# Performance work log

Measured on AMD Instinct MI355X. Metric: run time of the kernel, lower is better.

Reference implementation:

```python
import jax, jax.numpy as jnp
import numpy as np

N, D, H, O, P = 50000, 256, 512, 64, 1024


def setup_inputs() -> dict:
    key = jax.random.key(0)
    ks = jax.random.split(key, 9)
    x = jax.random.normal(ks[0], (N, D), dtype=jnp.float32)
    W1 = jax.random.normal(ks[1], (H, D), dtype=jnp.float32) / np.sqrt(D)
    b1 = jax.random.normal(ks[2], (H,), dtype=jnp.float32) * 0.01
    W2 = jax.random.normal(ks[3], (O, H), dtype=jnp.float32) / np.sqrt(H)
    b2 = jax.random.normal(ks[4], (O,), dtype=jnp.float32) * 0.01
    ap = jax.random.randint(ks[5], (P,), 0, N, dtype=jnp.int32)
    p = jax.random.randint(ks[6], (P,), 0, N, dtype=jnp.int32)
    an = jax.random.randint(ks[7], (P,), 0, N, dtype=jnp.int32)
    n = jax.random.randint(ks[8], (P,), 0, N, dtype=jnp.int32)
    return {"x": x, "W1": W1, "b1": b1, "W2": W2, "b2": b2,
            "ap": ap, "p": p, "an": an, "n": n}


def reference(x, W1, b1, W2, b2, ap, p, an, n):
    """ContrastiveHessianCalculator.compute_hessian, loss_func='contrastive_full',
    wrt='weight', shape='diagonal', speed='half' (exact GGN diag), for the nnj net
    Linear(D,H) -> Tanh -> Linear(H,O).

    For a pair (x1,x2) the combined diag m0 - 2*m1 + m2 equals
    diag((J1-J2)^T (J1-J2)) where Ji = d f(xi)/d params. Closed form per layer:
      W1[i,j]: S11_i*x1_j^2 - 2*S12_i*x1_j*x2_j + S22_i*x2_j^2,
               Sab_i = tanh'(z1a)_i * tanh'(z1b)_i * sum_o W2[o,i]^2
      b1[i]:   S11_i - 2*S12_i + S22_i
      W2[i,j]: (h1_j - h2_j)^2  (independent of output row i)
      b2[i]:   0  (bias Jacobians of the two branches cancel)
    Per-layer diags are flattened [weight, bias] and concatenated (torch.cat(.., dim=1)),
    then summed over the pair batch; return sum(pos) - sum(neg).
    """
    c = jnp.sum(W2 * W2, axis=0)  # [H]

    def pair_hess_diag(ia, ib):
        xa = x[ia]            # [P, D]
        xb = x[ib]            # [P, D]
        ha = jnp.tanh(xa @ W1.T + b1)   # [P, H]
        hb = jnp.tanh(xb @ W1.T + b1)
        da = 1.0 - ha * ha              # tanh' at x_a, [P, H]
        db = 1.0 - hb * hb
        S11 = da * da * c               # [P, H]
        S12 = da * db * c
        S22 = db * db * c
        # W1 diag: [P, H, D]
        W1d = (S11[:, :, None] * (xa * xa)[:, None, :]
               - 2.0 * S12[:, :, None] * (xa * xb)[:, None, :]
               + S22[:, :, None] * (xb * xb)[:, None, :])
        b1d = S11 - 2.0 * S12 + S22      # [P, H]
        hd = (ha - hb) ** 2              # [P, H]
        W2d = jnp.broadcast_to(hd[:, None, :], (hd.shape[0], O, H))  # [P, O, H]
        b2d = jnp.zeros((hd.shape[0], O), dtype=hd.dtype)
        flat = jnp.concatenate([W1d.reshape(hd.shape[0], -1), b1d,
                                W2d.reshape(hd.shape[0], -1), b2d], axis=1)
        return jnp.sum(flat, axis=0)     # sum over pair batch -> [n_params]

    pos = pair_hess_diag(ap, p)
    neg = pair_hess_diag(an, n)
    return pos - neg
```

## Files before the change

### kernel.cpp

```cpp
#include <hip/hip_runtime.h>
#include <math.h>

#define DD_ 256
#define HH_ 512
#define OO_ 64

typedef __attribute__((ext_vector_type(8))) short bf16x8s;
typedef __attribute__((ext_vector_type(4))) float f32x4;

__device__ __forceinline__ unsigned short f2bf(float f) {
    unsigned u = __float_as_uint(f);
    u += 0x7FFF + ((u >> 16) & 1);
    return (unsigned short)(u >> 16);
}
__device__ __forceinline__ float bf2f(unsigned short h) {
    return __uint_as_float(((unsigned)h) << 16);
}
__device__ __forceinline__ void conv8(const float4& v0, const float4& v1,
                                      bf16x8s& hi, bf16x8s& lo) {
    float f[8] = {v0.x, v0.y, v0.z, v0.w, v1.x, v1.y, v1.z, v1.w};
    #pragma unroll
    for (int e = 0; e < 8; ++e) {
        unsigned short hh = f2bf(f[e]);
        hi[e] = (short)hh;
        lo[e] = (short)f2bf(f[e] - bf2f(hh));
    }
}
__device__ __forceinline__ int swz8(int r, int s) {
    return s ^ (r & 7);
}

__global__ __launch_bounds__(256) void k_mega(
    const float* __restrict__ x, const float* __restrict__ W1,
    const float* __restrict__ b1, const float* __restrict__ W2,
    const int* __restrict__ ap, const int* __restrict__ pI,
    const int* __restrict__ an, const int* __restrict__ nI,
    short* __restrict__ Mt, short* __restrict__ Xt,
    float* __restrict__ pb1, float* __restrict__ phd) {
    const int t = threadIdx.x;
    const int bb = blockIdx.x;
    if (bb < 512) {
        __shared__ short Ah[64 * 64], Al[64 * 64], Bh[64 * 64], Bl[64 * 64];
        __shared__ float ht[64][67];
        __shared__ int sidx[64];
        const int n0 = (bb & 7) * 64;
        const int ry = bb >> 3;
        const int s = ry >> 5;
        const int p0 = (ry & 31) * 32;
        const int* IA = s ? an : ap;
        const int* IB = s ? nI : pI;
        if (t < 32) sidx[t] = IA[p0 + t];
        else if (t < 64) sidx[t] = IB[p0 + t - 32];
        __syncthreads();
        const int row = t >> 2, q = t & 3;
        const int l = t & 63, w = t >> 6;
        const int wm = w >> 1, wn = w & 1;
        const int lm = l & 15, g = l >> 4;
        const int sl0 = swz8(row, 2 * q) * 8;
        const int sl1 = swz8(row, 2 * q + 1) * 8;
        const float* srcA = x + (size_t)sidx[row] * DD_ + q * 16;
        const float* srcB = W1 + (size_t)(n0 + row) * DD_ + q * 16;
        f32x4 acc[2][2] = {};
        for (int ks = 0; ks < 4; ++ks) {
            const int k0 = ks * 64;
            {
                float4 a0 = *(const float4*)(srcA + k0);
                float4 a1 = *(const float4*)(srcA + k0 + 4);
                float4 a2 = *(const float4*)(srcA + k0 + 8);
                float4 a3 = *(const float4*)(srcA + k0 + 12);
                bf16x8s hi, lo;
                conv8(a0, a1, hi, lo);
                *(bf16x8s*)(&Ah[row * 64 + sl0]) = hi;
                *(bf16x8s*)(&Al[row * 64 + sl0]) = lo;
                conv8(a2, a3, hi, lo);
                *(bf16x8s*)(&Ah[row * 64 + sl1]) = hi;
                *(bf16x8s*)(&Al[row * 64 + sl1]) = lo;
            }
            {
                float4 b0 = *(const float4*)(srcB + k0);
                float4 b1q = *(const float4*)(srcB + k0 + 4);
                float4 b2 = *(const float4*)(srcB + k0 + 8);
                float4 b3 = *(const float4*)(srcB + k0 + 12);
                bf16x8s hi, lo;
                conv8(b0, b1q, hi, lo);
                *(bf16x8s*)(&Bh[row * 64 + sl0]) = hi;
                *(bf16x8s*)(&Bl[row * 64 + sl0]) = lo;
                conv8(b2, b3, hi, lo);
                *(bf16x8s*)(&Bh[row * 64 + sl1]) = hi;
                *(bf16x8s*)(&Bl[row * 64 + sl1]) = lo;
            }
            __syncthreads();
            #pragma unroll
            for (int kk = 0; kk < 2; ++kk) {
                bf16x8s ah[2], al[2], bh[2], bl[2];
                #pragma unroll
                for (int mi = 0; mi < 2; ++mi) {
                    int r = wm * 32 + mi * 16 + lm;
                    int off = r * 64 + swz8(r, kk * 4 + g) * 8;
                    ah[mi] = *(const bf16x8s*)(&Ah[off]);
                    al[mi] = *(const bf16x8s*)(&Al[off]);
                }
                #pragma unroll
                for (int nj = 0; nj < 2; ++nj) {
                    int r = wn * 32 + nj * 16 + lm;
                    int off = r * 64 + swz8(r, kk * 4 + g) * 8;
                    bh[nj] = *(const bf16x8s*)(&Bh[off]);
                    bl[nj] = *(const bf16x8s*)(&Bl[off]);
                }
                #pragma unroll
                for (int mi = 0; mi < 2; ++mi)
                    #pragma unroll
                    for (int nj = 0; nj < 2; ++nj) {
                        acc[mi][nj] = __builtin_amdgcn_mfma_f32_16x16x32_bf16(ah[mi], bh[nj], acc[mi][nj], 0, 0, 0);
                        acc[mi][nj] = __builtin_amdgcn_mfma_f32_16x16x32_bf16(ah[mi], bl[nj], acc[mi][nj], 0, 0, 0);
                        acc[mi][nj] = __builtin_amdgcn_mfma_f32_16x16x32_bf16(al[mi], bh[nj], acc[mi][nj], 0, 0, 0);
                    }
            }
            __syncthreads();
        }
        #pragma unroll
        for (int mi = 0; mi < 2; ++mi)
            #pragma unroll
            for (int nj = 0; nj < 2; ++nj) {
                int jl = wn * 32 + nj * 16 + lm;
                float bv = b1[n0 + jl];
                #pragma unroll
                for (int qq = 0; qq < 4; ++qq) {
                    int r = wm * 32 + mi * 16 + g * 4 + qq;
                    ht[r][jl] = tanhf(acc[mi][nj][qq] + bv);
                }
            }
        __syncthreads();
        const int il = t >> 2, pq = t & 3;
        float ci = 0.f;
        #pragma unroll 8
        for (int o = 0; o < OO_; ++o) { float wv = W2[o * HH_ + n0 + il]; ci += wv * wv; }
        const float sgn = s ? -1.f : 1.f;
        float b1p = 0.f, hdp = 0.f;
        bf16x8s v0, v1, v2;
        #pragma unroll
        for (int pp = 0; pp < 8; ++pp) {
            int pl = pq * 8 + pp;
            float ha = ht[pl][il];
            float hb = ht[pl + 32][il];
            float da = 1.f - ha * ha, db = 1.f - hb * hb;
            float s11 = sgn * (da * da * ci);
            float s12 = sgn * (-2.f * da * db * ci);
            float s22 = sgn * (db * db * ci);
            v0[pp] = (short)f2bf(s11);
            v1[pp] = (short)f2bf(s12);
            v2[pp] = (short)f2bf(s22);
            b1p += s11 + s12 + s22;
            float d = ha - hb;
            hdp += sgn * d * d;
        }
        size_t base = (size_t)(n0 + il) * 6144 + s * 1024 + p0 + pq * 8;
        *(bf16x8s*)(&Mt[base]) = v0;
        *(bf16x8s*)(&Mt[base + 2048]) = v1;
        *(bf16x8s*)(&Mt[base + 4096]) = v2;
        b1p += __shfl_xor(b1p, 1); b1p += __shfl_xor(b1p, 2);
        hdp += __shfl_xor(hdp, 1); hdp += __shfl_xor(hdp, 2);
        if (pq == 0) { pb1[ry * HH_ + n0 + il] = b1p; phd[ry * HH_ + n0 + il] = hdp; }
    } else {
        __shared__ int sia[64], sib[64];
        const int b2 = bb - 512;
        const int jblk = b2 >> 5, pblk = b2 & 31;
        const int j = jblk * 64 + (t >> 2), pq = t & 3;
        const int p0 = pblk * 64;
        const int s = p0 >> 10;
        const int* IA = s ? an : ap;
        const int* IB = s ? nI : pI;
        if (t < 64) sia[t] = IA[(p0 & 1023) + t];
        else if (t < 128) sib[t - 64] = IB[(p0 & 1023) + (t - 64)];
        __syncthreads();
        short xv[3][16];
        #pragma unroll
        for (int pp = 0; pp < 16; ++pp) {
            int pl = pq * 16 + pp;
            float xa = x[(size_t)sia[pl] * DD_ + j];
            float xb = x[(size_t)sib[pl] * DD_ + j];
            xv[0][pp] = (short)f2bf(xa * xa);
            xv[1][pp] = (short)f2bf(xa * xb);
            xv[2][pp] = (short)f2bf(xb * xb);
        }
        size_t base = (size_t)j * 6144 + p0 + pq * 16;
        #pragma unroll
        for (int term = 0; term < 3; ++term) {
            bf16x8s v0, v1;
            #pragma unroll
            for (int e = 0; e < 8; ++e) { v0[e] = xv[term][e]; v1[e] = xv[term][e + 8]; }
            *(bf16x8s*)(&Xt[base + (size_t)term * 2048]) = v0;
            *(bf16x8s*)(&Xt[base + (size_t)term * 2048 + 8]) = v1;
        }
    }
}

__global__ __launch_bounds__(256) void k_gemm2(
    const short* __restrict__ Mt, const short* __restrict__ Xt,
    float* __restrict__ part) {
    __shared__ short As[64 * 64], Bs[64 * 64];
    const int t = threadIdx.x;
    const int j0 = blockIdx.x * 64;
    const int i0 = blockIdx.y * 64;
    const int kb = blockIdx.z;
    const int row = t >> 2, q = t & 3;
    const int l = t & 63, w = t >> 6;
    const int wm = w >> 1, wn = w & 1;
    const int lm = l & 15, g = l >> 4;
    const int sl0 = swz8(row, 2 * q) * 8;
    const int sl1 = swz8(row, 2 * q + 1) * 8;
    const short* srcA = &Mt[(size_t)(i0 + row) * 6144 + kb * 384 + q * 16];
    const short* srcB = &Xt[(size_t)(j0 + row) * 6144 + kb * 384 + q * 16];
    f32x4 acc[2][2] = {};
    for (int ks = 0; ks < 6; ++ks) {
        const int k0 = ks * 64;
        *(bf16x8s*)(&As[row * 64 + sl0]) = *(const bf16x8s*)(srcA + k0);
        *(bf16x8s*)(&As[row * 64 + sl1]) = *(const bf16x8s*)(srcA + k0 + 8);
        *(bf16x8s*)(&Bs[row * 64 + sl0]) = *(const bf16x8s*)(srcB + k0);
        *(bf16x8s*)(&Bs[row * 64 + sl1]) = *(const bf16x8s*)(srcB + k0 + 8);
        __syncthreads();
        #pragma unroll
        for (int kk = 0; kk < 2; ++kk) {
            bf16x8s a[2], b[2];
            #pragma unroll
            for (int mi = 0; mi < 2; ++mi) {
                int r = wm * 32 + mi * 16 + lm;
                a[mi] = *(const bf16x8s*)(&As[r * 64 + swz8(r, kk * 4 + g) * 8]);
            }
            #pragma unroll
            for (int nj = 0; nj < 2; ++nj) {
                int r = wn * 32 + nj * 16 + lm;
                b[nj] = *(const bf16x8s*)(&Bs[r * 64 + swz8(r, kk * 4 + g) * 8]);
            }
            #pragma unroll
            for (int mi = 0; mi < 2; ++mi)
                #pragma unroll
                for (int nj = 0; nj < 2; ++nj)
                    acc[mi][nj] = __builtin_amdgcn_mfma_f32_16x16x32_bf16(a[mi], b[nj], acc[mi][nj], 0, 0, 0);
        }
        __syncthreads();
    }
    #pragma unroll
    for (int mi = 0; mi < 2; ++mi)
        #pragma unroll
        for (int nj = 0; nj < 2; ++nj) {
            int j = j0 + wn * 32 + nj * 16 + lm;
            #pragma unroll
            for (int qq = 0; qq < 4; ++qq) {
                int i = i0 + wm * 32 + mi * 16 + g * 4 + qq;
                part[((size_t)kb * HH_ + i) * DD_ + j] = acc[mi][nj][qq];
            }
        }
}

__global__ void k_tail(const float* __restrict__ part, const float* __restrict__ pb1,
                       const float* __restrict__ phd, float* __restrict__ out) {
    int gid = blockIdx.x * 256 + threadIdx.x;
    const int HD = HH_ * DD_;
    if (gid < HD) {
        float sv = 0.f;
        #pragma unroll
        for (int kb = 0; kb < 16; ++kb) sv += part[(size_t)kb * HD + gid];
        out[gid] = sv;
    } else if (gid < HD + HH_) {
        int i = gid - HD;
        float sv = 0.f;
        #pragma unroll
        for (int kb = 0; kb < 64; ++kb) sv += pb1[kb * HH_ + i];
        out[gid] = sv;
    } else if (gid < HD + HH_ + OO_ * HH_) {
        int i = (gid - HD - HH_) & (HH_ - 1);
        float sv = 0.f;
        #pragma unroll
        for (int kb = 0; kb < 64; ++kb) sv += phd[kb * HH_ + i];
        out[gid] = sv;
    } else if (gid < HD + HH_ + OO_ * HH_ + OO_) {
        out[gid] = 0.f;
    }
}

extern "C" void kernel_launch(void* const* d_in, const int* in_sizes, int n_in,
                              void* d_out, int out_size, void* d_ws, size_t ws_size,
                              hipStream_t stream) {
    const float* x  = (const float*)d_in[0];
    const float* W1 = (const float*)d_in[1];
    const float* b1 = (const float*)d_in[2];
    const float* W2 = (const float*)d_in[3];
    const int* ap = (const int*)d_in[5];
    const int* pI = (const int*)d_in[6];
    const int* an = (const int*)d_in[7];
    const int* nI = (const int*)d_in[8];
    float* out = (float*)d_out;
    float* ws = (float*)d_ws;

    float* part = ws;
    short* Mt   = (short*)(ws + 2097152);
    short* Xt   = (short*)(ws + 3670016);
    float* pb1  = ws + 4456448;
    float* phd  = ws + 4489216;

    k_mega<<<dim3(640), dim3(256), 0, stream>>>(x, W1, b1, W2, ap, pI, an, nI,
                                                Mt, Xt, pb1, phd);
    k_gemm2<<<dim3(4, 8, 16), dim3(256), 0, stream>>>(Mt, Xt, part);
    k_tail<<<dim3(643), dim3(256), 0, stream>>>(part, pb1, phd, out);
}
```

Baseline: 31.78 us.

## Fold Xt build into mega blocks, double split-K, vectorize tail reduction

The separate 128 blocks that built the Xt (x products) operand are removed. Each of the 512 GEMM1 blocks now also writes a quarter of an Xt tile after its own work, so the launch is uniform and 512 blocks wide. The second GEMM's split-K factor doubles from 16 to 32, halving the K per block to get more blocks in flight. The tail now reduces with float4 vectors, and one thread writes all 64 replicated W2 rows per vector. The costs are more partial-sum traffic (32 slices), a larger workspace, and Xt gathers that now read indices from global memory without an LDS stage.

```diff
diff --git a/kernel.cpp b/kernel.cpp
--- a/kernel.cpp
+++ b/kernel.cpp
@@ -6,6 +6,7 @@
 #define OO_ 64
 
 typedef __attribute__((ext_vector_type(8))) short bf16x8s;
+typedef __attribute__((ext_vector_type(4))) short bf16x4s;
 typedef __attribute__((ext_vector_type(4))) float f32x4;
 
 __device__ __forceinline__ unsigned short f2bf(float f) {
@@ -37,100 +38,100 @@
     const int* __restrict__ an, const int* __restrict__ nI,
     short* __restrict__ Mt, short* __restrict__ Xt,
     float* __restrict__ pb1, float* __restrict__ phd) {
+    __shared__ short Ah[64 * 64], Al[64 * 64], Bh[64 * 64], Bl[64 * 64];
+    __shared__ float ht[64][67];
+    __shared__ int sidx[64];
     const int t = threadIdx.x;
     const int bb = blockIdx.x;
-    if (bb < 512) {
-        __shared__ short Ah[64 * 64], Al[64 * 64], Bh[64 * 64], Bl[64 * 64];
-        __shared__ float ht[64][67];
-        __shared__ int sidx[64];
-        const int n0 = (bb & 7) * 64;
-        const int ry = bb >> 3;
-        const int s = ry >> 5;
-        const int p0 = (ry & 31) * 32;
-        const int* IA = s ? an : ap;
-        const int* IB = s ? nI : pI;
-        if (t < 32) sidx[t] = IA[p0 + t];
-        else if (t < 64) sidx[t] = IB[p0 + t - 32];
+    const int n0 = (bb & 7) * 64;
+    const int ry = bb >> 3;
+    const int s = ry >> 5;
+    const int p0 = (ry & 31) * 32;
+    const int* IA = s ? an : ap;
+    const int* IB = s ? nI : pI;
+    if (t < 32) sidx[t] = IA[p0 + t];
+    else if (t < 64) sidx[t] = IB[p0 + t - 32];
+    __syncthreads();
+    const int row = t >> 2, q = t & 3;
+    const int l = t & 63, w = t >> 6;
+    const int wm = w >> 1, wn = w & 1;
+    const int lm = l & 15, g = l >> 4;
+    const int sl0 = swz8(row, 2 * q) * 8;
+    const int sl1 = swz8(row, 2 * q + 1) * 8;
+    const float* srcA = x + (size_t)sidx[row] * DD_ + q * 16;
+    const float* srcB = W1 + (size_t)(n0 + row) * DD_ + q * 16;
+    f32x4 acc[2][2] = {};
+    for (int ks = 0; ks < 4; ++ks) {
+        const int k0 = ks * 64;
+        {
+            float4 a0 = *(const float4*)(srcA + k0);
+            float4 a1 = *(const float4*)(srcA + k0 + 4);
+            float4 a2 = *(const float4*)(srcA + k0 + 8);
+            float4 a3 = *(const float4*)(srcA + k0 + 12);
+            bf16x8s hi, lo;
+            conv8(a0, a1, hi, lo);
+            *(bf16x8s*)(&Ah[row * 64 + sl0]) = hi;
+            *(bf16x8s*)(&Al[row * 64 + sl0]) = lo;
+            conv8(a2, a3, hi, lo);
+            *(bf16x8s*)(&Ah[row * 64 + sl1]) = hi;
+            *(bf16x8s*)(&Al[row * 64 + sl1]) = lo;
+        }
+        {
+            float4 b0 = *(const float4*)(srcB + k0);
+            float4 b1q = *(const float4*)(srcB + k0 + 4);
+            float4 b2 = *(const float4*)(srcB + k0 + 8);
+            float4 b3 = *(const float4*)(srcB + k0 + 12);
+            bf16x8s hi, lo;
+            conv8(b0, b1q, hi, lo);
+            *(bf16x8s*)(&Bh[row * 64 + sl0]) = hi;
+            *(bf16x8s*)(&Bl[row * 64 + sl0]) = lo;
+            conv8(b2, b3, hi, lo);
+            *(bf16x8s*)(&Bh[row * 64 + sl1]) = hi;
+            *(bf16x8s*)(&Bl[row * 64 + sl1]) = lo;
+        }
         __syncthreads();
-        const int row = t >> 2, q = t & 3;
-        const int l = t & 63, w = t >> 6;
-        const int wm = w >> 1, wn = w & 1;
-        const int lm = l & 15, g = l >> 4;
-        const int sl0 = swz8(row, 2 * q) * 8;
-        const int sl1 = swz8(row, 2 * q + 1) * 8;
-        const float* srcA = x + (size_t)sidx[row] * DD_ + q * 16;
-        const float* srcB = W1 + (size_t)(n0 + row) * DD_ + q * 16;
-        f32x4 acc[2][2] = {};
-        for (int ks = 0; ks < 4; ++ks) {
-            const int k0 = ks * 64;
-            {
-                float4 a0 = *(const float4*)(srcA + k0);
-                float4 a1 = *(const float4*)(srcA + k0 + 4);
-                float4 a2 = *(const float4*)(srcA + k0 + 8);
-                float4 a3 = *(const float4*)(srcA + k0 + 12);
-                bf16x8s hi, lo;
-                conv8(a0, a1, hi, lo);
-                *(bf16x8s*)(&Ah[row * 64 + sl0]) = hi;
-                *(bf16x8s*)(&Al[row * 64 + sl0]) = lo;
-                conv8(a2, a3, hi, lo);
-                *(bf16x8s*)(&Ah[row * 64 + sl1]) = hi;
-                *(bf16x8s*)(&Al[row * 64 + sl1]) = lo;
-            }
-            {
-                float4 b0 = *(const float4*)(srcB + k0);
-                float4 b1q = *(const float4*)(srcB + k0 + 4);
-                float4 b2 = *(const float4*)(srcB + k0 + 8);
-                float4 b3 = *(const float4*)(srcB + k0 + 12);
-                bf16x8s hi, lo;
-                conv8(b0, b1q, hi, lo);
-                *(bf16x8s*)(&Bh[row * 64 + sl0]) = hi;
-                *(bf16x8s*)(&Bl[row * 64 + sl0]) = lo;
-                conv8(b2, b3, hi, lo);
-                *(bf16x8s*)(&Bh[row * 64 + sl1]) = hi;
-                *(bf16x8s*)(&Bl[row * 64 + sl1]) = lo;
-            }
-            __syncthreads();
-            #pragma unroll
-            for (int kk = 0; kk < 2; ++kk) {
-                bf16x8s ah[2], al[2], bh[2], bl[2];
-                #pragma unroll
-                for (int mi = 0; mi < 2; ++mi) {
-                    int r = wm * 32 + mi * 16 + lm;
-                    int off = r * 64 + swz8(r, kk * 4 + g) * 8;
-                    ah[mi] = *(const bf16x8s*)(&Ah[off]);
-                    al[mi] = *(const bf16x8s*)(&Al[off]);
-                }
+        #pragma unroll
+        for (int kk = 0; kk < 2; ++kk) {
+            bf16x8s ah[2], al[2], bh[2], bl[2];
+            #pragma unroll
+            for (int mi = 0; mi < 2; ++mi) {
+                int r = wm * 32 + mi * 16 + lm;
+                int off = r * 64 + swz8(r, kk * 4 + g) * 8;
+                ah[mi] = *(const bf16x8s*)(&Ah[off]);
+                al[mi] = *(const bf16x8s*)(&Al[off]);
+            }
+            #pragma unroll
+            for (int nj = 0; nj < 2; ++nj) {
+                int r = wn * 32 + nj * 16 + lm;
+                int off = r * 64 + swz8(r, kk * 4 + g) * 8;
+                bh[nj] = *(const bf16x8s*)(&Bh[off]);
+                bl[nj] = *(const bf16x8s*)(&Bl[off]);
+            }
+            #pragma unroll
+            for (int mi = 0; mi < 2; ++mi)
                 #pragma unroll
                 for (int nj = 0; nj < 2; ++nj) {
-                    int r = wn * 32 + nj * 16 + lm;
-                    int off = r * 64 + swz8(r, kk * 4 + g) * 8;
-                    bh[nj] = *(const bf16x8s*)(&Bh[off]);
-                    bl[nj] = *(const bf16x8s*)(&Bl[off]);
+                    acc[mi][nj] = __builtin_amdgcn_mfma_f32_16x16x32_bf16(ah[mi], bh[nj], acc[mi][nj], 0, 0, 0);
+                    acc[mi][nj] = __builtin_amdgcn_mfma_f32_16x16x32_bf16(ah[mi], bl[nj], acc[mi][nj], 0, 0, 0);
+                    acc[mi][nj] = __builtin_amdgcn_mfma_f32_16x16x32_bf16(al[mi], bh[nj], acc[mi][nj], 0, 0, 0);
                 }
-                #pragma unroll
-                for (int mi = 0; mi < 2; ++mi)
-                    #pragma unroll
-                    for (int nj = 0; nj < 2; ++nj) {
-                        acc[mi][nj] = __builtin_amdgcn_mfma_f32_16x16x32_bf16(ah[mi], bh[nj], acc[mi][nj], 0, 0, 0);
-                        acc[mi][nj] = __builtin_amdgcn_mfma_f32_16x16x32_bf16(ah[mi], bl[nj], acc[mi][nj], 0, 0, 0);
-                        acc[mi][nj] = __builtin_amdgcn_mfma_f32_16x16x32_bf16(al[mi], bh[nj], acc[mi][nj], 0, 0, 0);
-                    }
-            }
-            __syncthreads();
-        }
-        #pragma unroll
-        for (int mi = 0; mi < 2; ++mi)
-            #pragma unroll
-            for (int nj = 0; nj < 2; ++nj) {
-                int jl = wn * 32 + nj * 16 + lm;
-                float bv = b1[n0 + jl];
-                #pragma unroll
-                for (int qq = 0; qq < 4; ++qq) {
-                    int r = wm * 32 + mi * 16 + g * 4 + qq;
-                    ht[r][jl] = tanhf(acc[mi][nj][qq] + bv);
-                }
-            }
+        }
         __syncthreads();
+    }
+    #pragma unroll
+    for (int mi = 0; mi < 2; ++mi)
+        #pragma unroll
+        for (int nj = 0; nj < 2; ++nj) {
+            int jl = wn * 32 + nj * 16 + lm;
+            float bv = b1[n0 + jl];
+            #pragma unroll
+            for (int qq = 0; qq < 4; ++qq) {
+                int r = wm * 32 + mi * 16 + g * 4 + qq;
+                ht[r][jl] = tanhf(acc[mi][nj][qq] + bv);
+            }
+        }
+    __syncthreads();
+    {
         const int il = t >> 2, pq = t & 3;
         float ci = 0.f;
         #pragma unroll 8
@@ -161,36 +162,36 @@
         b1p += __shfl_xor(b1p, 1); b1p += __shfl_xor(b1p, 2);
         hdp += __shfl_xor(hdp, 1); hdp += __shfl_xor(hdp, 2);
         if (pq == 0) { pb1[ry * HH_ + n0 + il] = b1p; phd[ry * HH_ + n0 + il] = hdp; }
-    } else {
-        __shared__ int sia[64], sib[64];
-        const int b2 = bb - 512;
-        const int jblk = b2 >> 5, pblk = b2 & 31;
-        const int j = jblk * 64 + (t >> 2), pq = t & 3;
-        const int p0 = pblk * 64;
-        const int s = p0 >> 10;
-        const int* IA = s ? an : ap;
-        const int* IB = s ? nI : pI;
-        if (t < 64) sia[t] = IA[(p0 & 1023) + t];
-        else if (t < 128) sib[t - 64] = IB[(p0 & 1023) + (t - 64)];
-        __syncthreads();
-        short xv[3][16];
-        #pragma unroll
-        for (int pp = 0; pp < 16; ++pp) {
-            int pl = pq * 16 + pp;
-            float xa = x[(size_t)sia[pl] * DD_ + j];
-            float xb = x[(size_t)sib[pl] * DD_ + j];
+    }
+    {
+        const int xb = bb >> 2;
+        const int quarter = bb & 3;
+        const int jblk = xb >> 5, pblk = xb & 31;
+        const int j = jblk * 64 + (t >> 2);
+        const int pq = t & 3;
+        const int p0x = pblk * 64;
+        const int sX = p0x >> 10;
+        const int* IA2 = sX ? an : ap;
+        const int* IB2 = sX ? nI : pI;
+        const int pbase = (p0x & 1023) + quarter * 16 + pq * 4;
+        short xv[3][4];
+        #pragma unroll
+        for (int pp = 0; pp < 4; ++pp) {
+            int ia = IA2[pbase + pp];
+            int ib = IB2[pbase + pp];
+            float xa = x[(size_t)ia * DD_ + j];
+            float xbv = x[(size_t)ib * DD_ + j];
             xv[0][pp] = (short)f2bf(xa * xa);
-            xv[1][pp] = (short)f2bf(xa * xb);
-            xv[2][pp] = (short)f2bf(xb * xb);
-        }
-        size_t base = (size_t)j * 6144 + p0 + pq * 16;
+            xv[1][pp] = (short)f2bf(xa * xbv);
+            xv[2][pp] = (short)f2bf(xbv * xbv);
+        }
+        size_t base = (size_t)j * 6144 + p0x + quarter * 16 + pq * 4;
         #pragma unroll
         for (int term = 0; term < 3; ++term) {
-            bf16x8s v0, v1;
-            #pragma unroll
-            for (int e = 0; e < 8; ++e) { v0[e] = xv[term][e]; v1[e] = xv[term][e + 8]; }
-            *(bf16x8s*)(&Xt[base + (size_t)term * 2048]) = v0;
-            *(bf16x8s*)(&Xt[base + (size_t)term * 2048 + 8]) = v1;
+            bf16x4s v;
+            #pragma unroll
+            for (int e = 0; e < 4; ++e) v[e] = xv[term][e];
+            *(bf16x4s*)(&Xt[base + (size_t)term * 2048]) = v;
         }
     }
 }
@@ -209,10 +210,10 @@
     const int lm = l & 15, g = l >> 4;
     const int sl0 = swz8(row, 2 * q) * 8;
     const int sl1 = swz8(row, 2 * q + 1) * 8;
-    const short* srcA = &Mt[(size_t)(i0 + row) * 6144 + kb * 384 + q * 16];
-    const short* srcB = &Xt[(size_t)(j0 + row) * 6144 + kb * 384 + q * 16];
+    const short* srcA = &Mt[(size_t)(i0 + row) * 6144 + kb * 192 + q * 16];
+    const short* srcB = &Xt[(size_t)(j0 + row) * 6144 + kb * 192 + q * 16];
     f32x4 acc[2][2] = {};
-    for (int ks = 0; ks < 6; ++ks) {
+    for (int ks = 0; ks < 3; ++ks) {
         const int k0 = ks * 64;
         *(bf16x8s*)(&As[row * 64 + sl0]) = *(const bf16x8s*)(srcA + k0);
         *(bf16x8s*)(&As[row * 64 + sl1]) = *(const bf16x8s*)(srcA + k0 + 8);
@@ -255,27 +256,32 @@
 
 __global__ void k_tail(const float* __restrict__ part, const float* __restrict__ pb1,
                        const float* __restrict__ phd, float* __restrict__ out) {
-    int gid = blockIdx.x * 256 + threadIdx.x;
-    const int HD = HH_ * DD_;
-    if (gid < HD) {
-        float sv = 0.f;
-        #pragma unroll
-        for (int kb = 0; kb < 16; ++kb) sv += part[(size_t)kb * HD + gid];
-        out[gid] = sv;
-    } else if (gid < HD + HH_) {
-        int i = gid - HD;
-        float sv = 0.f;
-        #pragma unroll
-        for (int kb = 0; kb < 64; ++kb) sv += pb1[kb * HH_ + i];
-        out[gid] = sv;
-    } else if (gid < HD + HH_ + OO_ * HH_) {
-        int i = (gid - HD - HH_) & (HH_ - 1);
-        float sv = 0.f;
-        #pragma unroll
-        for (int kb = 0; kb < 64; ++kb) sv += phd[kb * HH_ + i];
-        out[gid] = sv;
-    } else if (gid < HD + HH_ + OO_ * HH_ + OO_) {
-        out[gid] = 0.f;
+    const int gid = blockIdx.x * 256 + threadIdx.x;
+    const int HD4 = 32768;
+    f32x4* out4 = (f32x4*)out;
+    if (gid < HD4) {
+        f32x4 sv = {};
+        #pragma unroll
+        for (int kb = 0; kb < 32; ++kb)
+            sv += *(const f32x4*)(&part[(size_t)kb * 131072 + gid * 4]);
+        out4[gid] = sv;
+    } else if (gid < HD4 + 128) {
+        const int i4 = gid - HD4;
+        f32x4 sv = {};
+        for (int k2 = 0; k2 < 64; ++k2)
+            sv += *(const f32x4*)(&pb1[k2 * HH_ + i4 * 4]);
+        out4[HD4 + i4] = sv;
+    } else if (gid < HD4 + 256) {
+        const int i4 = gid - HD4 - 128;
+        f32x4 sv = {};
+        for (int k2 = 0; k2 < 64; ++k2)
+            sv += *(const f32x4*)(&phd[k2 * HH_ + i4 * 4]);
+        #pragma unroll 8
+        for (int o = 0; o < OO_; ++o)
+            out4[HD4 + 128 + o * 128 + i4] = sv;
+    } else if (gid < HD4 + 272) {
+        f32x4 z = {};
+        out4[41088 + gid - HD4 - 256] = z;
     }
 }
 
@@ -294,13 +300,13 @@
     float* ws = (float*)d_ws;
 
     float* part = ws;
-    short* Mt   = (short*)(ws + 2097152);
-    short* Xt   = (short*)(ws + 3670016);
-    float* pb1  = ws + 4456448;
-    float* phd  = ws + 4489216;
-
-    k_mega<<<dim3(640), dim3(256), 0, stream>>>(x, W1, b1, W2, ap, pI, an, nI,
+    short* Mt   = (short*)(ws + 4194304);
+    short* Xt   = (short*)(ws + 5767168);
+    float* pb1  = ws + 6553600;
+    float* phd  = ws + 6586368;
+
+    k_mega<<<dim3(512), dim3(256), 0, stream>>>(x, W1, b1, W2, ap, pI, an, nI,
                                                 Mt, Xt, pb1, phd);
-    k_gemm2<<<dim3(4, 8, 16), dim3(256), 0, stream>>>(Mt, Xt, part);
-    k_tail<<<dim3(643), dim3(256), 0, stream>>>(part, pb1, phd, out);
-}
+    k_gemm2<<<dim3(4, 8, 32), dim3(256), 0, stream>>>(Mt, Xt, part);
+    k_tail<<<dim3(130), dim3(256), 0, stream>>>(part, pb1, phd, out);
+}
```

New measurement: 36.98 us. 1.16x slower.
